# Performance work log

Hardware: AMD Instinct MI355X
Metric: run time of the kernel (lower is better)

The kernel has to match this reference:

```python
import jax, jax.numpy as jnp
import numpy as np


def setup_inputs() -> dict:
    key = jax.random.key(0)
    k1, k2 = jax.random.split(key)
    x = jax.random.normal(k1, (32, 512, 384), dtype=jnp.float32)
    duration = jax.random.randint(k2, (32, 512), 0, 16, dtype=jnp.int32)
    return {"x": x, "duration": duration, "max_len": 4096}


def reference(x, duration, max_len):
    # x: [B, T, D] phoneme encodings; duration: [B, T] nonneg frame counts.
    # Equivalent to repeat_interleave(x, duration, axis=1) then pad/truncate to max_len.
    dur = jnp.maximum(duration, 0)
    cs = jnp.cumsum(dur, axis=1)                      # [B, T] cumulative end offsets
    t = jnp.arange(max_len, dtype=cs.dtype)          # [L] output frame positions
    # frame t belongs to phoneme i iff cs[i-1] <= t < cs[i]
    idx = jax.vmap(lambda c: jnp.searchsorted(c, t, side="right"))(cs)  # [B, L]
    total = cs[:, -1]                                 # [B] expanded lengths (mel_len)
    valid = t[None, :] < total[:, None]               # [B, L] frames beyond total are padding
    idx = jnp.minimum(idx, x.shape[1] - 1)
    out = jnp.take_along_axis(x, idx[:, :, None], axis=1)   # [B, L, D] gather
    out = jnp.where(valid[:, :, None], out, jnp.zeros((), dtype=x.dtype))
    return out, total
```

## Files before the change

### kernel.cpp

```cpp
#include <hip/hip_runtime.h>
#include <hip/hip_bf16.h>


#define B      32
#define S      512
#define T      4096
#define D      384
#define D4     96
#define TILE_T 64

__global__ __launch_bounds__(S) void lr_scan_kernel(
    const int* __restrict__ duration,
    int* __restrict__ cs,
    float* __restrict__ total_out)
{
    const int b   = blockIdx.x;
    const int tid = threadIdx.x;

    __shared__ int s[S];

    int d = duration[b * S + tid];
    d = max(d, 0);
    s[tid] = d;
    __syncthreads();

    #pragma unroll
    for (int off = 1; off < S; off <<= 1) {
        int v = (tid >= off) ? s[tid - off] : 0;
        __syncthreads();
        s[tid] += v;
        __syncthreads();
    }

    cs[b * S + tid] = s[tid];
    if (tid == 0) {
        total_out[b] = (float)s[S - 1];
    }
}

__global__ __launch_bounds__(256) void lr_gather_kernel(
    const float4* __restrict__ x,
    const int*    __restrict__ cs,
    float4*       __restrict__ out)
{
    const int blk = blockIdx.x;
    const int b   = blk >> 6;
    const int t0  = (blk & 63) * TILE_T;
    const int tid = threadIdx.x;

    __shared__ int s_cs[S];
    __shared__ int s_idx[TILE_T];

    s_cs[tid]       = cs[b * S + tid];
    s_cs[tid + 256] = cs[b * S + tid + 256];
    __syncthreads();

    const int total = s_cs[S - 1];

    if (tid < TILE_T) {
        const int t = t0 + tid;
        int idx = -1;
        if (t < total) {
            int lo = 0;
            #pragma unroll
            for (int step = 256; step > 0; step >>= 1) {
                int mid = lo + step;
                if (mid <= S && s_cs[mid - 1] <= t) lo = mid;
            }
            idx = min(lo, S - 1);
        }
        s_idx[tid] = idx;
    }
    __syncthreads();

    const float4* xb = x   + (size_t)b * S * D4;
    float4*       ob = out + ((size_t)b * T + t0) * D4;

    #pragma unroll 4
    for (int e = tid; e < TILE_T * D4; e += 256) {
        const int r = e / D4;
        const int c = e - r * D4;
        const int idx = s_idx[r];
        float4 v;
        if (idx < 0) {
            v = make_float4(0.f, 0.f, 0.f, 0.f);
        } else {
            v = xb[idx * D4 + c];
        }
        ob[r * D4 + c] = v;
    }
}

extern "C" void kernel_launch(void* const* d_in, const int* in_sizes, int n_in,
                              void* d_out, int out_size, void* d_ws, size_t ws_size,
                              hipStream_t stream) {
    const float* x        = (const float*)d_in[0];
    const int*   duration = (const int*)d_in[1];

    float* out      = (float*)d_out;
    float* total_of = out + (size_t)B * T * D;
    int*   cs       = (int*)d_ws;

    lr_scan_kernel<<<B, S, 0, stream>>>(duration, cs, total_of);

    const int nblocks = B * (T / TILE_T);
    lr_gather_kernel<<<nblocks, 256, 0, stream>>>(
        (const float4*)x, cs, (float4*)out);
}
```

Baseline: 44.66 us.

## Fuse duration prefix scan into gather kernel, dropping separate scan launch

```diff
diff --git a/kernel.cpp b/kernel.cpp
--- a/kernel.cpp
+++ b/kernel.cpp
@@ -9,39 +9,11 @@
 #define D4     96
 #define TILE_T 64
 
-__global__ __launch_bounds__(S) void lr_scan_kernel(
-    const int* __restrict__ duration,
-    int* __restrict__ cs,
-    float* __restrict__ total_out)
-{
-    const int b   = blockIdx.x;
-    const int tid = threadIdx.x;
-
-    __shared__ int s[S];
-
-    int d = duration[b * S + tid];
-    d = max(d, 0);
-    s[tid] = d;
-    __syncthreads();
-
-    #pragma unroll
-    for (int off = 1; off < S; off <<= 1) {
-        int v = (tid >= off) ? s[tid - off] : 0;
-        __syncthreads();
-        s[tid] += v;
-        __syncthreads();
-    }
-
-    cs[b * S + tid] = s[tid];
-    if (tid == 0) {
-        total_out[b] = (float)s[S - 1];
-    }
-}
-
-__global__ __launch_bounds__(256) void lr_gather_kernel(
+__global__ __launch_bounds__(256) void lr_fused_kernel(
     const float4* __restrict__ x,
-    const int*    __restrict__ cs,
-    float4*       __restrict__ out)
+    const int*    __restrict__ duration,
+    float4*       __restrict__ out,
+    float*        __restrict__ total_out)
 {
     const int blk = blockIdx.x;
     const int b   = blk >> 6;
@@ -49,13 +21,33 @@
     const int tid = threadIdx.x;
 
     __shared__ int s_cs[S];
+    __shared__ int s_p[256];
     __shared__ int s_idx[TILE_T];
 
-    s_cs[tid]       = cs[b * S + tid];
-    s_cs[tid + 256] = cs[b * S + tid + 256];
+    const int2 d2 = ((const int2*)(duration + b * S))[tid];
+    const int a0 = max(d2.x, 0);
+    const int a1 = max(d2.y, 0);
+    s_p[tid] = a0 + a1;
+    __syncthreads();
+
+    #pragma unroll
+    for (int off = 1; off < 256; off <<= 1) {
+        int v = (tid >= off) ? s_p[tid - off] : 0;
+        __syncthreads();
+        s_p[tid] += v;
+        __syncthreads();
+    }
+
+    const int P = s_p[tid];
+    s_cs[2 * tid]     = P - a1;
+    s_cs[2 * tid + 1] = P;
     __syncthreads();
 
     const int total = s_cs[S - 1];
+
+    if (t0 == 0 && tid == 0) {
+        total_out[b] = (float)total;
+    }
 
     if (tid < TILE_T) {
         const int t = t0 + tid;
@@ -99,11 +91,8 @@
 
     float* out      = (float*)d_out;
     float* total_of = out + (size_t)B * T * D;
-    int*   cs       = (int*)d_ws;
-
-    lr_scan_kernel<<<B, S, 0, stream>>>(duration, cs, total_of);
 
     const int nblocks = B * (T / TILE_T);
-    lr_gather_kernel<<<nblocks, 256, 0, stream>>>(
-        (const float4*)x, cs, (float4*)out);
+    lr_fused_kernel<<<nblocks, 256, 0, stream>>>(
+        (const float4*)x, duration, (float4*)out, total_of);
 }
```

Result: faster. 40.69 us (-8.9%).
